# Kernel tuning notes

Hardware: AMD Instinct MI355X
Metric: run time of the kernel (lower is better)

Reference implementation:

```python
import jax, jax.numpy as jnp
import numpy as np

N = 50000       # nodes
E = 600000      # edges (avg degree 12)
F_IN = 64       # input_bands
F_HID = 128     # 2 * input_bands
F_OUT = 128     # output_bands
EPS = 1e-5      # BatchNorm eps


def setup_inputs() -> dict:
    key = jax.random.key(0)
    ks = jax.random.split(key, 12)
    x = jax.random.normal(ks[0], (N, F_IN), jnp.float32)
    edge_index = jax.random.randint(ks[1], (2, E), 0, N, dtype=jnp.int32)
    # GCNConv weight (glorot-ish) and bias
    W1 = jax.random.normal(ks[2], (F_IN, F_HID), jnp.float32) / np.sqrt(F_IN)
    b1 = jnp.zeros((F_HID,), jnp.float32)
    gamma1 = jnp.ones((F_HID,), jnp.float32)
    beta1 = jnp.zeros((F_HID,), jnp.float32)
    # SAGEConv: lin_l (aggregated neighbors, with bias), lin_r (root, no bias)
    Wl = jax.random.normal(ks[3], (F_HID, F_OUT), jnp.float32) / np.sqrt(F_HID)
    bl = jnp.zeros((F_OUT,), jnp.float32)
    Wr = jax.random.normal(ks[4], (F_HID, F_OUT), jnp.float32) / np.sqrt(F_HID)
    gamma2 = jnp.ones((F_OUT,), jnp.float32)
    beta2 = jnp.zeros((F_OUT,), jnp.float32)
    return {"x": x, "edge_index": edge_index, "W1": W1, "b1": b1,
            "gamma1": gamma1, "beta1": beta1, "Wl": Wl, "bl": bl,
            "Wr": Wr, "gamma2": gamma2, "beta2": beta2}


def _bn_train(h, gamma, beta):
    # BatchNorm1d in training mode: biased batch stats over the node axis
    mean = h.mean(axis=0)
    var = h.var(axis=0)
    return gamma * (h - mean) * jax.lax.rsqrt(var + EPS) + beta


def _gcn_conv(x, src, dst, W, b):
    # PyG GCNConv: x' = D^{-1/2}(A + I)D^{-1/2} X W + b
    h = x @ W                                   # [N, F_HID]
    loop = jnp.arange(N, dtype=src.dtype)
    src_sl = jnp.concatenate([src, loop])       # self-loops appended
    dst_sl = jnp.concatenate([dst, loop])
    deg = jax.ops.segment_sum(jnp.ones(E + N, h.dtype), dst_sl, num_segments=N)
    dis = jnp.where(deg > 0, jax.lax.rsqrt(deg), 0.0)  # deg^{-1/2}, inf -> 0
    norm = dis[src_sl] * dis[dst_sl]            # [E+N]
    msg = h[src_sl] * norm[:, None]             # gather + scale
    return jax.ops.segment_sum(msg, dst_sl, num_segments=N) + b


def _sage_conv(x, src, dst, Wl, bl, Wr):
    # PyG SAGEConv (mean aggr): x' = lin_l(mean_{j in N(i)} x_j) + lin_r(x_i)
    cnt = jax.ops.segment_sum(jnp.ones(E, x.dtype), dst, num_segments=N)
    neigh = jax.ops.segment_sum(x[src], dst, num_segments=N)
    neigh = neigh / jnp.maximum(cnt, 1.0)[:, None]
    return neigh @ Wl + bl + x @ Wr


def reference(x, edge_index, W1, b1, gamma1, beta1, Wl, bl, Wr, gamma2, beta2):
    src, dst = edge_index[0], edge_index[1]
    h = _gcn_conv(x, src, dst, W1, b1)
    h = jax.nn.relu(_bn_train(h, gamma1, beta1))  # dropout = identity (eval)
    h = _sage_conv(h, src, dst, Wl, bl, Wr)
    h = jax.nn.relu(_bn_train(h, gamma2, beta2))
    return h
```

## Files before the change

### kernel.cpp

```cpp
#include <hip/hip_runtime.h>

#define NN 50000
#define NE 600000
#define FIN 64
#define FHID 128
#define BN_EPS 1e-5f
#define CAP 64

typedef __attribute__((ext_vector_type(8))) short short8;
typedef __attribute__((ext_vector_type(4))) float f32x4;

__device__ __forceinline__ unsigned short f2bf(float f) {
  unsigned u = __float_as_uint(f);
  return (unsigned short)((u + 0x7FFFu + ((u >> 16) & 1u)) >> 16);
}
__device__ __forceinline__ float bfs(unsigned short u) {
  return __uint_as_float(((unsigned)u) << 16);
}
__device__ __forceinline__ float bflo(unsigned v) { return __uint_as_float(v << 16); }
__device__ __forceinline__ float bfhi(unsigned v) { return __uint_as_float(v & 0xFFFF0000u); }
__device__ __forceinline__ unsigned pk2(float lo, float hi) {
  return (unsigned)f2bf(lo) | ((unsigned)f2bf(hi) << 16);
}

__global__ __launch_bounds__(256) void bucket_fill(const int* __restrict__ src,
                                                   const int* __restrict__ dst,
                                                   int* __restrict__ cnt,
                                                   int* __restrict__ csr) {
  int e4 = blockIdx.x * 256 + threadIdx.x;
  if (e4 * 4 < NE) {
    int4 d4 = ((const int4*)dst)[e4];
    int4 s4 = ((const int4*)src)[e4];
    int p;
    p = atomicAdd(&cnt[d4.x], 1); if (p < CAP) csr[(size_t)d4.x * CAP + p] = s4.x;
    p = atomicAdd(&cnt[d4.y], 1); if (p < CAP) csr[(size_t)d4.y * CAP + p] = s4.y;
    p = atomicAdd(&cnt[d4.z], 1); if (p < CAP) csr[(size_t)d4.z * CAP + p] = s4.z;
    p = atomicAdd(&cnt[d4.w], 1); if (p < CAP) csr[(size_t)d4.w * CAP + p] = s4.w;
  }
}

__global__ __launch_bounds__(256) void scale_x(const float* __restrict__ x,
                                               const int* __restrict__ cnt,
                                               ushort4* __restrict__ xs,
                                               int* __restrict__ csr) {
  int i = blockIdx.x * 256 + threadIdx.x;
  float4 v = ((const float4*)x)[i];
  int node = i >> 4;
  float d = rsqrtf((float)(cnt[node] + 1));
  xs[i] = make_ushort4(f2bf(v.x * d), f2bf(v.y * d), f2bf(v.z * d), f2bf(v.w * d));
  if (i < NN) {
    int deg = min(cnt[i], CAP);
    int deg8 = (deg + 7) & ~7;
    int* cb = csr + (size_t)i * CAP;
    for (int p = deg; p < deg8; ++p) cb[p] = 0;
  }
}

__device__ __forceinline__ void gacc(float& a0, float& a1, float& a2, float& a3,
                                     ushort4 v) {
  a0 += bfs(v.x); a1 += bfs(v.y); a2 += bfs(v.z); a3 += bfs(v.w);
}

__global__ __launch_bounds__(256) void gcn_agg(const unsigned short* __restrict__ xs,
                                               const int* __restrict__ csr,
                                               const int* __restrict__ cnt,
                                               unsigned short* __restrict__ xa) {
  int tid = threadIdx.x;
  int node = blockIdx.x * 16 + (tid >> 4);
  int li = tid & 15;
  int degr = cnt[node];
  int deg = min(degr, CAP);
  int deg8 = (deg + 7) & ~7;
  float di = rsqrtf((float)(degr + 1));
  ushort4 sv = *(const ushort4*)(xs + (size_t)node * FIN + li * 4);
  float a0 = bfs(sv.x), a1 = bfs(sv.y), a2 = bfs(sv.z), a3 = bfs(sv.w);
  ushort4 zv = *(const ushort4*)(xs + li * 4);
  const int* cb = csr + (size_t)node * CAP;
  int4 sA = *(const int4*)(cb);
  int4 sB = *(const int4*)(cb + 4);
  for (int e = 0; e < deg8; e += 8) {
    int pn = min(e + 8, CAP - 8);
    int4 nA = *(const int4*)(cb + pn);
    int4 nB = *(const int4*)(cb + pn + 4);
    ushort4 v0 = *(const ushort4*)(xs + (size_t)sA.x * FIN + li * 4);
    ushort4 v1 = *(const ushort4*)(xs + (size_t)sA.y * FIN + li * 4);
    ushort4 v2 = *(const ushort4*)(xs + (size_t)sA.z * FIN + li * 4);
    ushort4 v3 = *(const ushort4*)(xs + (size_t)sA.w * FIN + li * 4);
    ushort4 v4 = *(const ushort4*)(xs + (size_t)sB.x * FIN + li * 4);
    ushort4 v5 = *(const ushort4*)(xs + (size_t)sB.y * FIN + li * 4);
    ushort4 v6 = *(const ushort4*)(xs + (size_t)sB.z * FIN + li * 4);
    ushort4 v7 = *(const ushort4*)(xs + (size_t)sB.w * FIN + li * 4);
    gacc(a0, a1, a2, a3, v0); gacc(a0, a1, a2, a3, v1);
    gacc(a0, a1, a2, a3, v2); gacc(a0, a1, a2, a3, v3);
    gacc(a0, a1, a2, a3, v4); gacc(a0, a1, a2, a3, v5);
    gacc(a0, a1, a2, a3, v6); gacc(a0, a1, a2, a3, v7);
    sA = nA; sB = nB;
  }
  float pc = (float)(deg8 - deg);
  a0 -= pc * bfs(zv.x); a1 -= pc * bfs(zv.y);
  a2 -= pc * bfs(zv.z); a3 -= pc * bfs(zv.w);
  ushort4 o = make_ushort4(f2bf(di * a0), f2bf(di * a1), f2bf(di * a2), f2bf(di * a3));
  *(ushort4*)(xa + (size_t)node * FIN + li * 4) = o;
}

__device__ __forceinline__ void sacc(float* a, uint4 v) {
  a[0] += bflo(v.x); a[1] += bfhi(v.x);
  a[2] += bflo(v.y); a[3] += bfhi(v.y);
  a[4] += bflo(v.z); a[5] += bfhi(v.z);
  a[6] += bflo(v.w); a[7] += bfhi(v.w);
}

__global__ __launch_bounds__(256) void sage_agg(const unsigned* __restrict__ hb,
                                                const int* __restrict__ csr,
                                                const int* __restrict__ cnt,
                                                unsigned* __restrict__ neighb) {
  int tid = threadIdx.x;
  int node = blockIdx.x * 16 + (tid >> 4);
  int li = tid & 15;
  int degr = cnt[node];
  int deg = min(degr, CAP);
  int deg8 = (deg + 7) & ~7;
  float a[8];
#pragma unroll
  for (int i = 0; i < 8; ++i) a[i] = 0.f;
  uint4 zv = *(const uint4*)(hb + li * 4);
  const int* cb = csr + (size_t)node * CAP;
  int4 sA = *(const int4*)(cb);
  int4 sB = *(const int4*)(cb + 4);
  for (int e = 0; e < deg8; e += 8) {
    int pn = min(e + 8, CAP - 8);
    int4 nA = *(const int4*)(cb + pn);
    int4 nB = *(const int4*)(cb + pn + 4);
    uint4 v0 = *(const uint4*)(hb + (size_t)sA.x * 64 + li * 4);
    uint4 v1 = *(const uint4*)(hb + (size_t)sA.y * 64 + li * 4);
    uint4 v2 = *(const uint4*)(hb + (size_t)sA.z * 64 + li * 4);
    uint4 v3 = *(const uint4*)(hb + (size_t)sA.w * 64 + li * 4);
    uint4 v4 = *(const uint4*)(hb + (size_t)sB.x * 64 + li * 4);
    uint4 v5 = *(const uint4*)(hb + (size_t)sB.y * 64 + li * 4);
    uint4 v6 = *(const uint4*)(hb + (size_t)sB.z * 64 + li * 4);
    uint4 v7 = *(const uint4*)(hb + (size_t)sB.w * 64 + li * 4);
    sacc(a, v0); sacc(a, v1); sacc(a, v2); sacc(a, v3);
    sacc(a, v4); sacc(a, v5); sacc(a, v6); sacc(a, v7);
    sA = nA; sB = nB;
  }
  float pc = (float)(deg8 - deg);
  a[0] -= pc * bflo(zv.x); a[1] -= pc * bfhi(zv.x);
  a[2] -= pc * bflo(zv.y); a[3] -= pc * bfhi(zv.y);
  a[4] -= pc * bflo(zv.z); a[5] -= pc * bfhi(zv.z);
  a[6] -= pc * bflo(zv.w); a[7] -= pc * bfhi(zv.w);
  float inv = 1.0f / fmaxf((float)degr, 1.0f);
  uint4 o;
  o.x = pk2(a[0] * inv, a[1] * inv);
  o.y = pk2(a[2] * inv, a[3] * inv);
  o.z = pk2(a[4] * inv, a[5] * inv);
  o.w = pk2(a[6] * inv, a[7] * inv);
  *(uint4*)(neighb + (size_t)node * 64 + li * 4) = o;
}

template <int K1, int K2, bool OUTBF>
__global__ __launch_bounds__(256) void gemm_mfma(const short* __restrict__ A1,
                                                 const short* __restrict__ A2,
                                                 const float* __restrict__ B1,
                                                 const float* __restrict__ B2,
                                                 const float* __restrict__ bias,
                                                 float* __restrict__ Cf,
                                                 unsigned short* __restrict__ Cb,
                                                 float* __restrict__ sums,
                                                 float* __restrict__ sumsq) {
  constexpr int KT = K1 + K2;
  constexpr int NK1 = K1 / 32;
  constexpr int NKS = KT / 32;
  __shared__ short Bp[8 * NKS * 64 * 8];
  __shared__ float lsum[128], lsq[128];
  int tid = threadIdx.x;
  if (tid < 128) { lsum[tid] = 0.f; lsq[tid] = 0.f; }
  for (int idx = tid; idx < KT * 32; idx += 256) {
    int k = idx >> 5, c4 = idx & 31;
    const float* Bsrc = (K2 == 0 || k < K1) ? (B1 + k * 128) : (B2 + (k - K1) * 128);
    float4 wv = *(const float4*)(Bsrc + c4 * 4);
    int ks = k >> 5, q = (k >> 3) & 3, kk = k & 7;
#pragma unroll
    for (int j = 0; j < 4; ++j) {
      int c = c4 * 4 + j;
      int nf = c >> 4, r = c & 15;
      float wj = j == 0 ? wv.x : (j == 1 ? wv.y : (j == 2 ? wv.z : wv.w));
      Bp[((nf * NKS + ks) * 64 + q * 16 + r) * 8 + kk] = (short)f2bf(wj);
    }
  }
  __syncthreads();

  int lane = tid & 63;
  int w = tid >> 6;
  int r = lane & 15;
  int q = lane >> 4;
  int row_base = blockIdx.x * 128 + w * 32;
  int row0 = row_base + r;
  int row1 = row_base + 16 + r;
  row0 = row0 < NN ? row0 : NN - 1;
  row1 = row1 < NN ? row1 : NN - 1;

  short8 af[2][NKS];
#pragma unroll
  for (int ks = 0; ks < NKS; ++ks) {
    const short* A = (K2 == 0 || ks < NK1) ? A1 : A2;
    const int Kw = (K2 == 0 || ks < NK1) ? K1 : K2;
    const int ko = ((K2 == 0 || ks < NK1) ? ks : ks - NK1) * 32;
    af[0][ks] = *(const short8*)(A + (size_t)row0 * Kw + ko + q * 8);
    af[1][ks] = *(const short8*)(A + (size_t)row1 * Kw + ko + q * 8);
  }

  f32x4 acc[2][8];
#pragma unroll
  for (int m = 0; m < 2; ++m)
#pragma unroll
    for (int n = 0; n < 8; ++n) acc[m][n] = (f32x4){0.f, 0.f, 0.f, 0.f};

#pragma unroll
  for (int ks = 0; ks < NKS; ++ks) {
#pragma unroll
    for (int n = 0; n < 8; ++n) {
      short8 bf = *(const short8*)(Bp + ((size_t)(n * NKS + ks) * 64 + lane) * 8);
      acc[0][n] = __builtin_amdgcn_mfma_f32_16x16x32_bf16(af[0][ks], bf, acc[0][n], 0, 0, 0);
      acc[1][n] = __builtin_amdgcn_mfma_f32_16x16x32_bf16(af[1][ks], bf, acc[1][n], 0, 0, 0);
    }
  }

  float bias_r[8];
#pragma unroll
  for (int n = 0; n < 8; ++n) bias_r[n] = bias[n * 16 + r];
  float cs[8], cq[8];
#pragma unroll
  for (int n = 0; n < 8; ++n) { cs[n] = 0.f; cq[n] = 0.f; }
#pragma unroll
  for (int m = 0; m < 2; ++m)
#pragma unroll
    for (int i = 0; i < 4; ++i) {
      int row = row_base + m * 16 + q * 4 + i;
      if (row < NN) {
#pragma unroll
        for (int n = 0; n < 8; ++n) {
          float v = acc[m][n][i] + bias_r[n];
          int col = n * 16 + r;
          if constexpr (OUTBF)
            Cb[(size_t)row * 128 + col] = f2bf(v);
          else
            Cf[(size_t)row * 128 + col] = v;
          cs[n] += v;
          cq[n] += v * v;
        }
      }
    }
#pragma unroll
  for (int n = 0; n < 8; ++n) {
    atomicAdd(&lsum[n * 16 + r], cs[n]);
    atomicAdd(&lsq[n * 16 + r], cq[n]);
  }
  __syncthreads();
  if (tid < 128) {
    atomicAdd(&sums[tid], lsum[tid]);
    atomicAdd(&sumsq[tid], lsq[tid]);
  }
}

__global__ __launch_bounds__(256) void bn_apply_bf(unsigned* __restrict__ hb,
                                                   const float* __restrict__ sums,
                                                   const float* __restrict__ sumsq,
                                                   const float* __restrict__ gamma,
                                                   const float* __restrict__ beta) {
  __shared__ float sc[128], sh[128];
  int t = threadIdx.x;
  if (t < 128) {
    float mean = sums[t] * (1.0f / NN);
    float var = fmaxf(sumsq[t] * (1.0f / NN) - mean * mean, 0.f);
    float inv = rsqrtf(var + BN_EPS);
    float s = gamma[t] * inv;
    sc[t] = s;
    sh[t] = beta[t] - mean * s;
  }
  __syncthreads();
  int i = blockIdx.x * 256 + t;
  uint2 v = ((uint2*)hb)[i];
  int c = (i & 31) * 4;
  float f0 = fmaxf(fmaf(bflo(v.x), sc[c + 0], sh[c + 0]), 0.f);
  float f1 = fmaxf(fmaf(bfhi(v.x), sc[c + 1], sh[c + 1]), 0.f);
  float f2 = fmaxf(fmaf(bflo(v.y), sc[c + 2], sh[c + 2]), 0.f);
  float f3 = fmaxf(fmaf(bfhi(v.y), sc[c + 3], sh[c + 3]), 0.f);
  v.x = (unsigned)f2bf(f0) | ((unsigned)f2bf(f1) << 16);
  v.y = (unsigned)f2bf(f2) | ((unsigned)f2bf(f3) << 16);
  ((uint2*)hb)[i] = v;
}

__global__ __launch_bounds__(256) void bn_apply_f32(float* __restrict__ out,
                                                    const float* __restrict__ sums,
                                                    const float* __restrict__ sumsq,
                                                    const float* __restrict__ gamma,
                                                    const float* __restrict__ beta) {
  __shared__ float sc[128], sh[128];
  int t = threadIdx.x;
  if (t < 128) {
    float mean = sums[t] * (1.0f / NN);
    float var = fmaxf(sumsq[t] * (1.0f / NN) - mean * mean, 0.f);
    float inv = rsqrtf(var + BN_EPS);
    float s = gamma[t] * inv;
    sc[t] = s;
    sh[t] = beta[t] - mean * s;
  }
  __syncthreads();
  int i4 = blockIdx.x * 256 + t;
  float4 v = ((const float4*)out)[i4];
  int f = (i4 & 31) * 4;
  v.x = fmaxf(fmaf(v.x, sc[f + 0], sh[f + 0]), 0.f);
  v.y = fmaxf(fmaf(v.y, sc[f + 1], sh[f + 1]), 0.f);
  v.z = fmaxf(fmaf(v.z, sc[f + 2], sh[f + 2]), 0.f);
  v.w = fmaxf(fmaf(v.w, sc[f + 3], sh[f + 3]), 0.f);
  ((float4*)out)[i4] = v;
}

extern "C" void kernel_launch(void* const* d_in, const int* in_sizes, int n_in,
                              void* d_out, int out_size, void* d_ws, size_t ws_size,
                              hipStream_t stream) {
  const float* x   = (const float*)d_in[0];
  const int*   ei  = (const int*)d_in[1];
  const float* W1  = (const float*)d_in[2];
  const float* b1  = (const float*)d_in[3];
  const float* g1  = (const float*)d_in[4];
  const float* be1 = (const float*)d_in[5];
  const float* Wl  = (const float*)d_in[6];
  const float* bl  = (const float*)d_in[7];
  const float* Wr  = (const float*)d_in[8];
  const float* g2  = (const float*)d_in[9];
  const float* be2 = (const float*)d_in[10];
  const int* srcp = ei;
  const int* dstp = ei + NE;

  char* w = (char*)d_ws;
  auto alloc = [&](size_t bytes) {
    char* p = w;
    w += (bytes + 255) & ~(size_t)255;
    return p;
  };
  int*   cnt     = (int*)alloc((size_t)NN * 4);
  int*   csr     = (int*)alloc((size_t)NN * CAP * 4);
  unsigned short* xs     = (unsigned short*)alloc((size_t)NN * FIN * 2);
  unsigned short* xa     = (unsigned short*)alloc((size_t)NN * FIN * 2);
  unsigned short* hb     = (unsigned short*)alloc((size_t)NN * FHID * 2);
  unsigned*       neighb = (unsigned*)alloc((size_t)NN * FHID * 2);
  float* stats   = (float*)alloc(8 * 128 * 4);
  float* sums1 = stats,       *sumsq1 = stats + 128;
  float* sums2 = stats + 512, *sumsq2 = stats + 640;

  hipMemsetAsync(cnt, 0, (size_t)NN * 4, stream);
  hipMemsetAsync(stats, 0, 8 * 128 * 4, stream);

  int nbE4 = (NE / 4 + 255) / 256;
  int nbA = NN / 16;
  int nbG = (NN + 127) / 128;

  bucket_fill<<<nbE4, 256, 0, stream>>>(srcp, dstp, cnt, csr);
  scale_x<<<NN * FIN / 4 / 256, 256, 0, stream>>>(x, cnt, (ushort4*)xs, csr);

  gcn_agg<<<nbA, 256, 0, stream>>>(xs, csr, cnt, xa);
  gemm_mfma<64, 0, true><<<nbG, 256, 0, stream>>>(
      (const short*)xa, nullptr, W1, nullptr, b1, nullptr, hb, sums1, sumsq1);
  bn_apply_bf<<<NN * FHID / 4 / 256, 256, 0, stream>>>((unsigned*)hb, sums1, sumsq1,
                                                       g1, be1);

  sage_agg<<<nbA, 256, 0, stream>>>((const unsigned*)hb, csr, cnt, neighb);
  gemm_mfma<128, 128, false><<<nbG, 256, 0, stream>>>(
      (const short*)neighb, (const short*)hb, Wl, Wr, bl, (float*)d_out, nullptr,
      sums2, sumsq2);
  bn_apply_f32<<<NN * FHID / 4 / 256, 256, 0, stream>>>((float*)d_out, sums2, sumsq2,
                                                        g2, be2);
}
```

Before: 234.6 us.

## Fuse graph aggregation with MFMA GEMMs and fold BN1 into SAGE gather

Merges the GCN aggregation with its GEMM and the SAGE aggregation with its GEMM, staging aggregated rows in shared memory instead of writing them to global buffers. The first BatchNorm+ReLU is applied on the fly during the SAGE gather and the root-feature load, which removes the bn_apply_bf pass. Weight packing to bf16 MFMA layout moves into extra blocks of the bucket_fill kernel, and the two memsets become one. This cuts launches and intermediate HBM traffic but recomputes BN+ReLU per gathered neighbor and lowers per-block GEMM tile height.

Result: slower. 245.1 us (+4.5%).

```diff
diff --git a/kernel.cpp b/kernel.cpp
--- a/kernel.cpp
+++ b/kernel.cpp
@@ -1,4 +1,5 @@
 #include <hip/hip_runtime.h>
+
 
 #define NN 50000
 #define NE 600000
@@ -23,19 +24,40 @@
   return (unsigned)f2bf(lo) | ((unsigned)f2bf(hi) << 16);
 }
 
-__global__ __launch_bounds__(256) void bucket_fill(const int* __restrict__ src,
-                                                   const int* __restrict__ dst,
-                                                   int* __restrict__ cnt,
-                                                   int* __restrict__ csr) {
-  int e4 = blockIdx.x * 256 + threadIdx.x;
-  if (e4 * 4 < NE) {
-    int4 d4 = ((const int4*)dst)[e4];
-    int4 s4 = ((const int4*)src)[e4];
-    int p;
-    p = atomicAdd(&cnt[d4.x], 1); if (p < CAP) csr[(size_t)d4.x * CAP + p] = s4.x;
-    p = atomicAdd(&cnt[d4.y], 1); if (p < CAP) csr[(size_t)d4.y * CAP + p] = s4.y;
-    p = atomicAdd(&cnt[d4.z], 1); if (p < CAP) csr[(size_t)d4.z * CAP + p] = s4.z;
-    p = atomicAdd(&cnt[d4.w], 1); if (p < CAP) csr[(size_t)d4.w * CAP + p] = s4.w;
+__global__ __launch_bounds__(256) void bucket_fill(
+    const int* __restrict__ src, const int* __restrict__ dst,
+    int* __restrict__ cnt, int* __restrict__ csr,
+    const float* __restrict__ W1, const float* __restrict__ Wl,
+    const float* __restrict__ Wr, short* __restrict__ Wp1,
+    short* __restrict__ Wp2, int nbE4) {
+  int tid = threadIdx.x;
+  if ((int)blockIdx.x < nbE4) {
+    int e4 = blockIdx.x * 256 + tid;
+    if (e4 * 4 < NE) {
+      int4 d4 = ((const int4*)dst)[e4];
+      int4 s4 = ((const int4*)src)[e4];
+      int p;
+      p = atomicAdd(&cnt[d4.x], 1); if (p < CAP) csr[(size_t)d4.x * CAP + p] = s4.x;
+      p = atomicAdd(&cnt[d4.y], 1); if (p < CAP) csr[(size_t)d4.y * CAP + p] = s4.y;
+      p = atomicAdd(&cnt[d4.z], 1); if (p < CAP) csr[(size_t)d4.z * CAP + p] = s4.z;
+      p = atomicAdd(&cnt[d4.w], 1); if (p < CAP) csr[(size_t)d4.w * CAP + p] = s4.w;
+    }
+  } else {
+    int widx = (blockIdx.x - nbE4) * 256 + tid;
+    if (widx < 8192) {
+      int kk = widx & 7, lane = (widx >> 3) & 63, ks = (widx >> 9) & 1,
+          n = widx >> 10;
+      int q = lane >> 4, r = lane & 15;
+      int k = ks * 32 + q * 8 + kk, col = n * 16 + r;
+      Wp1[widx] = (short)f2bf(W1[k * 128 + col]);
+    } else if (widx < 8192 + 32768) {
+      int w2 = widx - 8192;
+      int kk = w2 & 7, lane = (w2 >> 3) & 63, ks = (w2 >> 9) & 7, n = w2 >> 12;
+      int q = lane >> 4, r = lane & 15;
+      int k = ks * 32 + q * 8 + kk, col = n * 16 + r;
+      float wv = (k < 128) ? Wl[k * 128 + col] : Wr[(k - 128) * 128 + col];
+      Wp2[w2] = (short)f2bf(wv);
+    }
   }
 }
 
@@ -61,195 +83,93 @@
   a0 += bfs(v.x); a1 += bfs(v.y); a2 += bfs(v.z); a3 += bfs(v.w);
 }
 
-__global__ __launch_bounds__(256) void gcn_agg(const unsigned short* __restrict__ xs,
-                                               const int* __restrict__ csr,
-                                               const int* __restrict__ cnt,
-                                               unsigned short* __restrict__ xa) {
-  int tid = threadIdx.x;
-  int node = blockIdx.x * 16 + (tid >> 4);
-  int li = tid & 15;
-  int degr = cnt[node];
-  int deg = min(degr, CAP);
-  int deg8 = (deg + 7) & ~7;
-  float di = rsqrtf((float)(degr + 1));
-  ushort4 sv = *(const ushort4*)(xs + (size_t)node * FIN + li * 4);
-  float a0 = bfs(sv.x), a1 = bfs(sv.y), a2 = bfs(sv.z), a3 = bfs(sv.w);
-  ushort4 zv = *(const ushort4*)(xs + li * 4);
-  const int* cb = csr + (size_t)node * CAP;
-  int4 sA = *(const int4*)(cb);
-  int4 sB = *(const int4*)(cb + 4);
-  for (int e = 0; e < deg8; e += 8) {
-    int pn = min(e + 8, CAP - 8);
-    int4 nA = *(const int4*)(cb + pn);
-    int4 nB = *(const int4*)(cb + pn + 4);
-    ushort4 v0 = *(const ushort4*)(xs + (size_t)sA.x * FIN + li * 4);
-    ushort4 v1 = *(const ushort4*)(xs + (size_t)sA.y * FIN + li * 4);
-    ushort4 v2 = *(const ushort4*)(xs + (size_t)sA.z * FIN + li * 4);
-    ushort4 v3 = *(const ushort4*)(xs + (size_t)sA.w * FIN + li * 4);
-    ushort4 v4 = *(const ushort4*)(xs + (size_t)sB.x * FIN + li * 4);
-    ushort4 v5 = *(const ushort4*)(xs + (size_t)sB.y * FIN + li * 4);
-    ushort4 v6 = *(const ushort4*)(xs + (size_t)sB.z * FIN + li * 4);
-    ushort4 v7 = *(const ushort4*)(xs + (size_t)sB.w * FIN + li * 4);
-    gacc(a0, a1, a2, a3, v0); gacc(a0, a1, a2, a3, v1);
-    gacc(a0, a1, a2, a3, v2); gacc(a0, a1, a2, a3, v3);
-    gacc(a0, a1, a2, a3, v4); gacc(a0, a1, a2, a3, v5);
-    gacc(a0, a1, a2, a3, v6); gacc(a0, a1, a2, a3, v7);
-    sA = nA; sB = nB;
-  }
-  float pc = (float)(deg8 - deg);
-  a0 -= pc * bfs(zv.x); a1 -= pc * bfs(zv.y);
-  a2 -= pc * bfs(zv.z); a3 -= pc * bfs(zv.w);
-  ushort4 o = make_ushort4(f2bf(di * a0), f2bf(di * a1), f2bf(di * a2), f2bf(di * a3));
-  *(ushort4*)(xa + (size_t)node * FIN + li * 4) = o;
-}
-
-__device__ __forceinline__ void sacc(float* a, uint4 v) {
-  a[0] += bflo(v.x); a[1] += bfhi(v.x);
-  a[2] += bflo(v.y); a[3] += bfhi(v.y);
-  a[4] += bflo(v.z); a[5] += bfhi(v.z);
-  a[6] += bflo(v.w); a[7] += bfhi(v.w);
-}
-
-__global__ __launch_bounds__(256) void sage_agg(const unsigned* __restrict__ hb,
-                                                const int* __restrict__ csr,
-                                                const int* __restrict__ cnt,
-                                                unsigned* __restrict__ neighb) {
-  int tid = threadIdx.x;
-  int node = blockIdx.x * 16 + (tid >> 4);
-  int li = tid & 15;
-  int degr = cnt[node];
-  int deg = min(degr, CAP);
-  int deg8 = (deg + 7) & ~7;
-  float a[8];
-#pragma unroll
-  for (int i = 0; i < 8; ++i) a[i] = 0.f;
-  uint4 zv = *(const uint4*)(hb + li * 4);
-  const int* cb = csr + (size_t)node * CAP;
-  int4 sA = *(const int4*)(cb);
-  int4 sB = *(const int4*)(cb + 4);
-  for (int e = 0; e < deg8; e += 8) {
-    int pn = min(e + 8, CAP - 8);
-    int4 nA = *(const int4*)(cb + pn);
-    int4 nB = *(const int4*)(cb + pn + 4);
-    uint4 v0 = *(const uint4*)(hb + (size_t)sA.x * 64 + li * 4);
-    uint4 v1 = *(const uint4*)(hb + (size_t)sA.y * 64 + li * 4);
-    uint4 v2 = *(const uint4*)(hb + (size_t)sA.z * 64 + li * 4);
-    uint4 v3 = *(const uint4*)(hb + (size_t)sA.w * 64 + li * 4);
-    uint4 v4 = *(const uint4*)(hb + (size_t)sB.x * 64 + li * 4);
-    uint4 v5 = *(const uint4*)(hb + (size_t)sB.y * 64 + li * 4);
-    uint4 v6 = *(const uint4*)(hb + (size_t)sB.z * 64 + li * 4);
-    uint4 v7 = *(const uint4*)(hb + (size_t)sB.w * 64 + li * 4);
-    sacc(a, v0); sacc(a, v1); sacc(a, v2); sacc(a, v3);
-    sacc(a, v4); sacc(a, v5); sacc(a, v6); sacc(a, v7);
-    sA = nA; sB = nB;
-  }
-  float pc = (float)(deg8 - deg);
-  a[0] -= pc * bflo(zv.x); a[1] -= pc * bfhi(zv.x);
-  a[2] -= pc * bflo(zv.y); a[3] -= pc * bfhi(zv.y);
-  a[4] -= pc * bflo(zv.z); a[5] -= pc * bfhi(zv.z);
-  a[6] -= pc * bflo(zv.w); a[7] -= pc * bfhi(zv.w);
-  float inv = 1.0f / fmaxf((float)degr, 1.0f);
-  uint4 o;
-  o.x = pk2(a[0] * inv, a[1] * inv);
-  o.y = pk2(a[2] * inv, a[3] * inv);
-  o.z = pk2(a[4] * inv, a[5] * inv);
-  o.w = pk2(a[6] * inv, a[7] * inv);
-  *(uint4*)(neighb + (size_t)node * 64 + li * 4) = o;
-}
-
-template <int K1, int K2, bool OUTBF>
-__global__ __launch_bounds__(256) void gemm_mfma(const short* __restrict__ A1,
-                                                 const short* __restrict__ A2,
-                                                 const float* __restrict__ B1,
-                                                 const float* __restrict__ B2,
-                                                 const float* __restrict__ bias,
-                                                 float* __restrict__ Cf,
-                                                 unsigned short* __restrict__ Cb,
-                                                 float* __restrict__ sums,
-                                                 float* __restrict__ sumsq) {
-  constexpr int KT = K1 + K2;
-  constexpr int NK1 = K1 / 32;
-  constexpr int NKS = KT / 32;
-  __shared__ short Bp[8 * NKS * 64 * 8];
+__global__ __launch_bounds__(256) void gcn_block(
+    const unsigned short* __restrict__ xs, const int* __restrict__ csr,
+    const int* __restrict__ cnt, const short* __restrict__ Wp1,
+    const float* __restrict__ b1, unsigned short* __restrict__ hb,
+    float* __restrict__ sums1, float* __restrict__ sumsq1) {
+  __shared__ unsigned short xaS[64][72];
   __shared__ float lsum[128], lsq[128];
   int tid = threadIdx.x;
   if (tid < 128) { lsum[tid] = 0.f; lsq[tid] = 0.f; }
-  for (int idx = tid; idx < KT * 32; idx += 256) {
-    int k = idx >> 5, c4 = idx & 31;
-    const float* Bsrc = (K2 == 0 || k < K1) ? (B1 + k * 128) : (B2 + (k - K1) * 128);
-    float4 wv = *(const float4*)(Bsrc + c4 * 4);
-    int ks = k >> 5, q = (k >> 3) & 3, kk = k & 7;
-#pragma unroll
-    for (int j = 0; j < 4; ++j) {
-      int c = c4 * 4 + j;
-      int nf = c >> 4, r = c & 15;
-      float wj = j == 0 ? wv.x : (j == 1 ? wv.y : (j == 2 ? wv.z : wv.w));
-      Bp[((nf * NKS + ks) * 64 + q * 16 + r) * 8 + kk] = (short)f2bf(wj);
-    }
-  }
-  __syncthreads();
-
-  int lane = tid & 63;
-  int w = tid >> 6;
-  int r = lane & 15;
-  int q = lane >> 4;
-  int row_base = blockIdx.x * 128 + w * 32;
-  int row0 = row_base + r;
-  int row1 = row_base + 16 + r;
-  row0 = row0 < NN ? row0 : NN - 1;
-  row1 = row1 < NN ? row1 : NN - 1;
-
-  short8 af[2][NKS];
-#pragma unroll
-  for (int ks = 0; ks < NKS; ++ks) {
-    const short* A = (K2 == 0 || ks < NK1) ? A1 : A2;
-    const int Kw = (K2 == 0 || ks < NK1) ? K1 : K2;
-    const int ko = ((K2 == 0 || ks < NK1) ? ks : ks - NK1) * 32;
-    af[0][ks] = *(const short8*)(A + (size_t)row0 * Kw + ko + q * 8);
-    af[1][ks] = *(const short8*)(A + (size_t)row1 * Kw + ko + q * 8);
-  }
-
-  f32x4 acc[2][8];
-#pragma unroll
-  for (int m = 0; m < 2; ++m)
-#pragma unroll
-    for (int n = 0; n < 8; ++n) acc[m][n] = (f32x4){0.f, 0.f, 0.f, 0.f};
-
-#pragma unroll
-  for (int ks = 0; ks < NKS; ++ks) {
+  int row_base = blockIdx.x * 64;
+  int li = tid & 15, g = tid >> 4;
+  ushort4 zv = *(const ushort4*)(xs + li * 4);
+  for (int it = 0; it < 4; ++it) {
+    int lr = g * 4 + it;
+    int node = row_base + lr;
+    if (node < NN) {
+      int degr = cnt[node];
+      int deg = min(degr, CAP);
+      int deg8 = (deg + 7) & ~7;
+      float di = rsqrtf((float)(degr + 1));
+      ushort4 sv = *(const ushort4*)(xs + (size_t)node * FIN + li * 4);
+      float a0 = bfs(sv.x), a1 = bfs(sv.y), a2 = bfs(sv.z), a3 = bfs(sv.w);
+      const int* cb = csr + (size_t)node * CAP;
+      int4 sA = *(const int4*)(cb);
+      int4 sB = *(const int4*)(cb + 4);
+      for (int e = 0; e < deg8; e += 8) {
+        int pn = min(e + 8, CAP - 8);
+        int4 nA = *(const int4*)(cb + pn);
+        int4 nB = *(const int4*)(cb + pn + 4);
+        ushort4 v0 = *(const ushort4*)(xs + (size_t)sA.x * FIN + li * 4);
+        ushort4 v1 = *(const ushort4*)(xs + (size_t)sA.y * FIN + li * 4);
+        ushort4 v2 = *(const ushort4*)(xs + (size_t)sA.z * FIN + li * 4);
+        ushort4 v3 = *(const ushort4*)(xs + (size_t)sA.w * FIN + li * 4);
+        ushort4 v4 = *(const ushort4*)(xs + (size_t)sB.x * FIN + li * 4);
+        ushort4 v5 = *(const ushort4*)(xs + (size_t)sB.y * FIN + li * 4);
+        ushort4 v6 = *(const ushort4*)(xs + (size_t)sB.z * FIN + li * 4);
+        ushort4 v7 = *(const ushort4*)(xs + (size_t)sB.w * FIN + li * 4);
+        gacc(a0, a1, a2, a3, v0); gacc(a0, a1, a2, a3, v1);
+        gacc(a0, a1, a2, a3, v2); gacc(a0, a1, a2, a3, v3);
+        gacc(a0, a1, a2, a3, v4); gacc(a0, a1, a2, a3, v5);
+        gacc(a0, a1, a2, a3, v6); gacc(a0, a1, a2, a3, v7);
+        sA = nA; sB = nB;
+      }
+      float pc = (float)(deg8 - deg);
+      a0 -= pc * bfs(zv.x); a1 -= pc * bfs(zv.y);
+      a2 -= pc * bfs(zv.z); a3 -= pc * bfs(zv.w);
+      *(ushort4*)(&xaS[lr][li * 4]) = make_ushort4(
+          f2bf(di * a0), f2bf(di * a1), f2bf(di * a2), f2bf(di * a3));
+    }
+  }
+  __syncthreads();
+
+  int lane = tid & 63, w = tid >> 6, r = lane & 15, q = lane >> 4;
+  short8 af[2];
+#pragma unroll
+  for (int ks = 0; ks < 2; ++ks)
+    af[ks] = *(const short8*)(&xaS[w * 16 + r][ks * 32 + q * 8]);
+  f32x4 acc[8];
+#pragma unroll
+  for (int n = 0; n < 8; ++n) acc[n] = (f32x4){0.f, 0.f, 0.f, 0.f};
+#pragma unroll
+  for (int ks = 0; ks < 2; ++ks)
 #pragma unroll
     for (int n = 0; n < 8; ++n) {
-      short8 bf = *(const short8*)(Bp + ((size_t)(n * NKS + ks) * 64 + lane) * 8);
-      acc[0][n] = __builtin_amdgcn_mfma_f32_16x16x32_bf16(af[0][ks], bf, acc[0][n], 0, 0, 0);
-      acc[1][n] = __builtin_amdgcn_mfma_f32_16x16x32_bf16(af[1][ks], bf, acc[1][n], 0, 0, 0);
-    }
-  }
+      short8 bf = *(const short8*)(Wp1 + ((size_t)(n * 2 + ks) * 64 + lane) * 8);
+      acc[n] = __builtin_amdgcn_mfma_f32_16x16x32_bf16(af[ks], bf, acc[n], 0, 0, 0);
+    }
 
   float bias_r[8];
 #pragma unroll
-  for (int n = 0; n < 8; ++n) bias_r[n] = bias[n * 16 + r];
+  for (int n = 0; n < 8; ++n) bias_r[n] = b1[n * 16 + r];
   float cs[8], cq[8];
 #pragma unroll
   for (int n = 0; n < 8; ++n) { cs[n] = 0.f; cq[n] = 0.f; }
 #pragma unroll
-  for (int m = 0; m < 2; ++m)
-#pragma unroll
-    for (int i = 0; i < 4; ++i) {
-      int row = row_base + m * 16 + q * 4 + i;
-      if (row < NN) {
-#pragma unroll
-        for (int n = 0; n < 8; ++n) {
-          float v = acc[m][n][i] + bias_r[n];
-          int col = n * 16 + r;
-          if constexpr (OUTBF)
-            Cb[(size_t)row * 128 + col] = f2bf(v);
-          else
-            Cf[(size_t)row * 128 + col] = v;
-          cs[n] += v;
-          cq[n] += v * v;
-        }
+  for (int i = 0; i < 4; ++i) {
+    int row = row_base + w * 16 + q * 4 + i;
+    if (row < NN) {
+#pragma unroll
+      for (int n = 0; n < 8; ++n) {
+        float v = acc[n][i] + bias_r[n];
+        hb[(size_t)row * 128 + n * 16 + r] = f2bf(v);
+        cs[n] += v;
+        cq[n] += v * v;
       }
     }
+  }
 #pragma unroll
   for (int n = 0; n < 8; ++n) {
     atomicAdd(&lsum[n * 16 + r], cs[n]);
@@ -257,37 +177,161 @@
   }
   __syncthreads();
   if (tid < 128) {
-    atomicAdd(&sums[tid], lsum[tid]);
-    atomicAdd(&sumsq[tid], lsq[tid]);
-  }
-}
-
-__global__ __launch_bounds__(256) void bn_apply_bf(unsigned* __restrict__ hb,
-                                                   const float* __restrict__ sums,
-                                                   const float* __restrict__ sumsq,
-                                                   const float* __restrict__ gamma,
-                                                   const float* __restrict__ beta) {
-  __shared__ float sc[128], sh[128];
-  int t = threadIdx.x;
-  if (t < 128) {
-    float mean = sums[t] * (1.0f / NN);
-    float var = fmaxf(sumsq[t] * (1.0f / NN) - mean * mean, 0.f);
-    float inv = rsqrtf(var + BN_EPS);
-    float s = gamma[t] * inv;
-    sc[t] = s;
-    sh[t] = beta[t] - mean * s;
-  }
-  __syncthreads();
-  int i = blockIdx.x * 256 + t;
-  uint2 v = ((uint2*)hb)[i];
-  int c = (i & 31) * 4;
-  float f0 = fmaxf(fmaf(bflo(v.x), sc[c + 0], sh[c + 0]), 0.f);
-  float f1 = fmaxf(fmaf(bfhi(v.x), sc[c + 1], sh[c + 1]), 0.f);
-  float f2 = fmaxf(fmaf(bflo(v.y), sc[c + 2], sh[c + 2]), 0.f);
-  float f3 = fmaxf(fmaf(bfhi(v.y), sc[c + 3], sh[c + 3]), 0.f);
-  v.x = (unsigned)f2bf(f0) | ((unsigned)f2bf(f1) << 16);
-  v.y = (unsigned)f2bf(f2) | ((unsigned)f2bf(f3) << 16);
-  ((uint2*)hb)[i] = v;
+    atomicAdd(&sums1[tid], lsum[tid]);
+    atomicAdd(&sumsq1[tid], lsq[tid]);
+  }
+}
+
+__device__ __forceinline__ void sbn(float* a, uint4 v, const float* sc,
+                                    const float* sh) {
+  a[0] += fmaxf(fmaf(bflo(v.x), sc[0], sh[0]), 0.f);
+  a[1] += fmaxf(fmaf(bfhi(v.x), sc[1], sh[1]), 0.f);
+  a[2] += fmaxf(fmaf(bflo(v.y), sc[2], sh[2]), 0.f);
+  a[3] += fmaxf(fmaf(bfhi(v.y), sc[3], sh[3]), 0.f);
+  a[4] += fmaxf(fmaf(bflo(v.z), sc[4], sh[4]), 0.f);
+  a[5] += fmaxf(fmaf(bfhi(v.z), sc[5], sh[5]), 0.f);
+  a[6] += fmaxf(fmaf(bflo(v.w), sc[6], sh[6]), 0.f);
+  a[7] += fmaxf(fmaf(bfhi(v.w), sc[7], sh[7]), 0.f);
+}
+
+__global__ __launch_bounds__(256) void sage_block(
+    const unsigned short* __restrict__ hb, const int* __restrict__ csr,
+    const int* __restrict__ cnt, const short* __restrict__ Wp2,
+    const float* __restrict__ bl, const float* __restrict__ sums1,
+    const float* __restrict__ sumsq1, const float* __restrict__ g1,
+    const float* __restrict__ be1, float* __restrict__ out,
+    float* __restrict__ sums2, float* __restrict__ sumsq2) {
+  __shared__ unsigned short nbS[64][136];
+  __shared__ float scB[128], shB[128], lsum[128], lsq[128];
+  int tid = threadIdx.x;
+  if (tid < 128) {
+    lsum[tid] = 0.f; lsq[tid] = 0.f;
+    float mean = sums1[tid] * (1.0f / NN);
+    float var = fmaxf(sumsq1[tid] * (1.0f / NN) - mean * mean, 0.f);
+    float s = g1[tid] * rsqrtf(var + BN_EPS);
+    scB[tid] = s;
+    shB[tid] = be1[tid] - mean * s;
+  }
+  __syncthreads();
+
+  int row_base = blockIdx.x * 64;
+  int li = tid & 15, g = tid >> 4;
+  const unsigned* hbu = (const unsigned*)hb;
+  float sc8[8], sh8[8];
+#pragma unroll
+  for (int j = 0; j < 8; ++j) { sc8[j] = scB[li * 8 + j]; sh8[j] = shB[li * 8 + j]; }
+  float zb[8];
+  {
+    uint4 zr = *(const uint4*)(hbu + li * 4);
+    float t[8] = {0,0,0,0,0,0,0,0};
+    sbn(t, zr, sc8, sh8);
+#pragma unroll
+    for (int j = 0; j < 8; ++j) zb[j] = t[j];
+  }
+  for (int it = 0; it < 4; ++it) {
+    int lr = g * 4 + it;
+    int node = row_base + lr;
+    if (node < NN) {
+      int degr = cnt[node];
+      int deg = min(degr, CAP);
+      int deg8 = (deg + 7) & ~7;
+      float a[8];
+#pragma unroll
+      for (int j = 0; j < 8; ++j) a[j] = 0.f;
+      const int* cb = csr + (size_t)node * CAP;
+      int4 sA = *(const int4*)(cb);
+      int4 sB = *(const int4*)(cb + 4);
+      for (int e = 0; e < deg8; e += 8) {
+        int pn = min(e + 8, CAP - 8);
+        int4 nA = *(const int4*)(cb + pn);
+        int4 nB = *(const int4*)(cb + pn + 4);
+        uint4 v0 = *(const uint4*)(hbu + (size_t)sA.x * 64 + li * 4);
+        uint4 v1 = *(const uint4*)(hbu + (size_t)sA.y * 64 + li * 4);
+        uint4 v2 = *(const uint4*)(hbu + (size_t)sA.z * 64 + li * 4);
+        uint4 v3 = *(const uint4*)(hbu + (size_t)sA.w * 64 + li * 4);
+        uint4 v4 = *(const uint4*)(hbu + (size_t)sB.x * 64 + li * 4);
+        uint4 v5 = *(const uint4*)(hbu + (size_t)sB.y * 64 + li * 4);
+        uint4 v6 = *(const uint4*)(hbu + (size_t)sB.z * 64 + li * 4);
+        uint4 v7 = *(const uint4*)(hbu + (size_t)sB.w * 64 + li * 4);
+        sbn(a, v0, sc8, sh8); sbn(a, v1, sc8, sh8);
+        sbn(a, v2, sc8, sh8); sbn(a, v3, sc8, sh8);
+        sbn(a, v4, sc8, sh8); sbn(a, v5, sc8, sh8);
+        sbn(a, v6, sc8, sh8); sbn(a, v7, sc8, sh8);
+        sA = nA; sB = nB;
+      }
+      float pc = (float)(deg8 - deg);
+#pragma unroll
+      for (int j = 0; j < 8; ++j) a[j] -= pc * zb[j];
+      float inv = 1.0f / fmaxf((float)degr, 1.0f);
+      uint4 o;
+      o.x = pk2(a[0] * inv, a[1] * inv);
+      o.y = pk2(a[2] * inv, a[3] * inv);
+      o.z = pk2(a[4] * inv, a[5] * inv);
+      o.w = pk2(a[6] * inv, a[7] * inv);
+      *(uint4*)(&nbS[lr][li * 8]) = o;
+    }
+  }
+  __syncthreads();
+
+  int lane = tid & 63, w = tid >> 6, r = lane & 15, q = lane >> 4;
+  int rowg = row_base + w * 16 + r;
+  rowg = rowg < NN ? rowg : NN - 1;
+  short8 af[8];
+#pragma unroll
+  for (int ks = 0; ks < 4; ++ks)
+    af[ks] = *(const short8*)(&nbS[w * 16 + r][ks * 32 + q * 8]);
+#pragma unroll
+  for (int ks = 4; ks < 8; ++ks) {
+    int kg = (ks - 4) * 32 + q * 8;
+    short8 raw = *(const short8*)((const short*)hb + (size_t)rowg * 128 + kg);
+    short8 t;
+#pragma unroll
+    for (int j = 0; j < 8; ++j) {
+      float f = fmaxf(fmaf(bfs((unsigned short)raw[j]), scB[kg + j], shB[kg + j]), 0.f);
+      t[j] = (short)f2bf(f);
+    }
+    af[ks] = t;
+  }
+  f32x4 acc[8];
+#pragma unroll
+  for (int n = 0; n < 8; ++n) acc[n] = (f32x4){0.f, 0.f, 0.f, 0.f};
+#pragma unroll
+  for (int ks = 0; ks < 8; ++ks)
+#pragma unroll
+    for (int n = 0; n < 8; ++n) {
+      short8 bf = *(const short8*)(Wp2 + ((size_t)(n * 8 + ks) * 64 + lane) * 8);
+      acc[n] = __builtin_amdgcn_mfma_f32_16x16x32_bf16(af[ks], bf, acc[n], 0, 0, 0);
+    }
+
+  float bias_r[8];
+#pragma unroll
+  for (int n = 0; n < 8; ++n) bias_r[n] = bl[n * 16 + r];
+  float cs[8], cq[8];
+#pragma unroll
+  for (int n = 0; n < 8; ++n) { cs[n] = 0.f; cq[n] = 0.f; }
+#pragma unroll
+  for (int i = 0; i < 4; ++i) {
+    int row = row_base + w * 16 + q * 4 + i;
+    if (row < NN) {
+#pragma unroll
+      for (int n = 0; n < 8; ++n) {
+        float v = acc[n][i] + bias_r[n];
+        out[(size_t)row * 128 + n * 16 + r] = v;
+        cs[n] += v;
+        cq[n] += v * v;
+      }
+    }
+  }
+#pragma unroll
+  for (int n = 0; n < 8; ++n) {
+    atomicAdd(&lsum[n * 16 + r], cs[n]);
+    atomicAdd(&lsq[n * 16 + r], cq[n]);
+  }
+  __syncthreads();
+  if (tid < 128) {
+    atomicAdd(&sums2[tid], lsum[tid]);
+    atomicAdd(&sumsq2[tid], lsq[tid]);
+  }
 }
 
 __global__ __launch_bounds__(256) void bn_apply_f32(float* __restrict__ out,
@@ -339,36 +383,31 @@
     w += (bytes + 255) & ~(size_t)255;
     return p;
   };
-  int*   cnt     = (int*)alloc((size_t)NN * 4);
-  int*   csr     = (int*)alloc((size_t)NN * CAP * 4);
-  unsigned short* xs     = (unsigned short*)alloc((size_t)NN * FIN * 2);
-  unsigned short* xa     = (unsigned short*)alloc((size_t)NN * FIN * 2);
-  unsigned short* hb     = (unsigned short*)alloc((size_t)NN * FHID * 2);
-  unsigned*       neighb = (unsigned*)alloc((size_t)NN * FHID * 2);
-  float* stats   = (float*)alloc(8 * 128 * 4);
+  size_t zbytes = (NN + 1024) * 4;
+  char* zz = (char*)alloc(zbytes);
+  int*   cnt   = (int*)zz;
+  float* stats = (float*)(cnt + NN);
   float* sums1 = stats,       *sumsq1 = stats + 128;
   float* sums2 = stats + 512, *sumsq2 = stats + 640;
 
-  hipMemsetAsync(cnt, 0, (size_t)NN * 4, stream);
-  hipMemsetAsync(stats, 0, 8 * 128 * 4, stream);
+  int*   csr = (int*)alloc((size_t)NN * CAP * 4);
+  unsigned short* xs = (unsigned short*)alloc((size_t)NN * FIN * 2);
+  unsigned short* hb = (unsigned short*)alloc((size_t)NN * FHID * 2);
+  short* Wp1 = (short*)alloc(8192 * 2);
+  short* Wp2 = (short*)alloc(32768 * 2);
+
+  hipMemsetAsync(zz, 0, zbytes, stream);
 
   int nbE4 = (NE / 4 + 255) / 256;
-  int nbA = NN / 16;
-  int nbG = (NN + 127) / 128;
-
-  bucket_fill<<<nbE4, 256, 0, stream>>>(srcp, dstp, cnt, csr);
+  int nbW  = (8192 + 32768 + 255) / 256;
+  int nb64 = (NN + 63) / 64;
+
+  bucket_fill<<<nbE4 + nbW, 256, 0, stream>>>(srcp, dstp, cnt, csr, W1, Wl, Wr,
+                                              Wp1, Wp2, nbE4);
   scale_x<<<NN * FIN / 4 / 256, 256, 0, stream>>>(x, cnt, (ushort4*)xs, csr);
-
-  gcn_agg<<<nbA, 256, 0, stream>>>(xs, csr, cnt, xa);
-  gemm_mfma<64, 0, true><<<nbG, 256, 0, stream>>>(
-      (const short*)xa, nullptr, W1, nullptr, b1, nullptr, hb, sums1, sumsq1);
-  bn_apply_bf<<<NN * FHID / 4 / 256, 256, 0, stream>>>((unsigned*)hb, sums1, sumsq1,
-                                                       g1, be1);
-
-  sage_agg<<<nbA, 256, 0, stream>>>((const unsigned*)hb, csr, cnt, neighb);
-  gemm_mfma<128, 128, false><<<nbG, 256, 0, stream>>>(
-      (const short*)neighb, (const short*)hb, Wl, Wr, bl, (float*)d_out, nullptr,
-      sums2, sumsq2);
-  bn_apply_f32<<<NN * FHID / 4 / 256, 256, 0, stream>>>((float*)d_out, sums2, sumsq2,
-                                                        g2, be2);
-}
+  gcn_block<<<nb64, 256, 0, stream>>>(xs, csr, cnt, Wp1, b1, hb, sums1, sumsq1);
+  sage_block<<<nb64, 256, 0, stream>>>(hb, csr, cnt, Wp2, bl, sums1, sumsq1,
+                                       g1, be1, (float*)d_out, sums2, sumsq2);
+  bn_apply_f32<<<NN * FHID / 4 / 256, 256, 0, stream>>>((float*)d_out, sums2,
+                                                        sumsq2, g2, be2);
+}
```
